# Kernel optimization log

Measured on AMD Instinct MI355X. Metric: run time of the kernel, lower is better.

## Reference

```python
import jax, jax.numpy as jnp
import numpy as np

B, T, I, H = 128, 1024, 128, 512


def setup_inputs():
    key = jax.random.key(0)
    ks = jax.random.split(key, 7)
    x = jax.random.normal(ks[0], (B, T, I), jnp.float32)
    mask = (jax.random.uniform(ks[1], (B, T)) < 0.1).astype(jnp.int32)
    # lengths sorted DESCENDING (required by the per-step batch truncation); max == T
    length = jnp.sort(jax.random.randint(ks[2], (B,), T // 2, T + 1))[::-1]
    length = length.at[0].set(T)
    s = 1.0 / np.sqrt(H)
    W_ih = jax.random.uniform(ks[3], (4 * H, I), jnp.float32, -s, s)
    W_hh = jax.random.uniform(ks[4], (4 * H, H), jnp.float32, -s, s)
    b_ih = jax.random.uniform(ks[5], (4 * H,), jnp.float32, -s, s)
    b_hh = jax.random.uniform(ks[6], (4 * H,), jnp.float32, -s, s)
    return dict(input=x, mask=mask, length=length, W_ih=W_ih, W_hh=W_hh, b_ih=b_ih, b_hh=b_hh)


def _boundary_mask(mask, length):
    # mask[:,0]=0 then scatter 1 at end index (length-1), as in the torch code
    Bq = mask.shape[0]
    m = mask.astype(jnp.float32)
    m = m.at[:, 0].set(0.0)
    m = m.at[jnp.arange(Bq), length - 1].set(1.0)
    return m


def _gather_index(m):
    # Replicates the pad-to-max-words while-loop + nonzero/gather pipeline.
    # The loop extends a suffix of ones until each row has exactly max_w ones;
    # equivalently: set to 1 every position whose suffix zero-count <= (max_w - num).
    Bq, Tq = m.shape
    word_nums = m.sum(axis=1)
    max_w = word_nums.max()
    need = max_w - word_nums
    zcum = jnp.cumsum((1.0 - m)[:, ::-1], axis=1)[:, ::-1]  # zeros in suffix (inclusive)
    padded = jnp.where(zcum <= need[:, None], 1.0, m)
    K = int(max_w)  # every row now has exactly K ones
    # column indices of the ones, in ascending order (row-major nonzero order)
    cols = jnp.argsort(1.0 - padded, axis=1, stable=True)[:, :K]
    # index = row*T + col - 1, gathered from the flattened embeddings (torch wraps -1)
    flat_idx = (jnp.arange(Bq)[:, None] * Tq + cols - 1) % (Bq * Tq)
    return flat_idx, word_nums, K


def _run_lstm(x, m, active, W_ih, W_hh, b_ih, b_hh):
    # Masked per-timestep LSTMCell: h,c are zeroed at boundaries (mask==0) before
    # each step; rows with t >= length are frozen (emulates batch_size_t truncation
    # for descending-sorted lengths) and their embeddings stay zero.
    Bq = x.shape[0]
    Hq = W_hh.shape[1]
    h0 = jnp.zeros((Bq, Hq), x.dtype)

    def step(carry, xs):
        h, c = carry
        x_t, m_t, a_t = xs
        h = h * m_t[:, None]
        c = c * m_t[:, None]
        gates = x_t @ W_ih.T + h @ W_hh.T + b_ih + b_hh
        i, f, g, o = jnp.split(gates, 4, axis=1)  # torch gate order i,f,g,o
        c2 = jax.nn.sigmoid(f) * c + jax.nn.sigmoid(i) * jnp.tanh(g)
        h2 = jax.nn.sigmoid(o) * jnp.tanh(c2)
        a = a_t[:, None]
        return (a * h2 + (1.0 - a) * h, a * c2 + (1.0 - a) * c), a * h2

    _, emb = jax.lax.scan(step, (h0, h0), (x.transpose(1, 0, 2), m.T, active.T))
    return emb.transpose(1, 0, 2)  # [B, T, H]


def reference(input, mask, length, W_ih, W_hh, b_ih, b_hh):
    Bq, Tq, _ = input.shape
    Hq = W_hh.shape[1]
    m = _boundary_mask(mask, length)
    active = (jnp.arange(Tq)[None, :] < length[:, None]).astype(input.dtype)
    emb = _run_lstm(input, m, active, W_ih, W_hh, b_ih, b_hh)
    flat_idx, word_nums, K = _gather_index(m)
    out = emb.reshape(Bq * Tq, Hq)[flat_idx]  # [B, K, H]
    return out, word_nums
```

## Files before the change

### kernel.cpp

```cpp
#include <hip/hip_runtime.h>
#include <math.h>

#define BB 128
#define TT 1024
#define II 128
#define HH 512
#define GG 2048
#define BT (BB*TT)
#define LMAX 10
#define NBUCK 12

#define BM 128
#define BN 128
#define KCH 128

typedef unsigned short u16;
typedef __attribute__((ext_vector_type(4))) u16 u16x4;
typedef __attribute__((ext_vector_type(8))) u16 u16x8;
typedef __attribute__((ext_vector_type(8))) short bf16x8;
typedef __attribute__((ext_vector_type(4))) float f32x4;

typedef __attribute__((address_space(3))) unsigned int lds_u32;
typedef __attribute__((address_space(1))) const unsigned int gbl_u32;

__device__ __forceinline__ void gload16(const void* g, void* l) {
    __builtin_amdgcn_global_load_lds((gbl_u32*)g, (lds_u32*)l, 16, 0, 0);
}

__device__ __forceinline__ float rcpf(float x) { return __builtin_amdgcn_rcpf(x); }
__device__ __forceinline__ float sigf(float v) { return rcpf(1.0f + __expf(-v)); }
__device__ __forceinline__ float tanhfast(float x) {
    float e = __expf(2.0f * x);
    return 1.0f - 2.0f * rcpf(e + 1.0f);
}

__device__ __forceinline__ u16 f2b(float f) {
    unsigned int x = __float_as_uint(f);
    return (u16)((x + 0x7fffu + ((x >> 16) & 1u)) >> 16);
}

__host__ __device__ __forceinline__ void buck_geom(int bkt, int CAP0, int* off, int* cap) {
    if (bkt == 0) { *off = 0; *cap = CAP0; return; }
    int o = CAP0;
    if (bkt == 1) { *off = o; *cap = 2048; return; } o += 2048;
    if (bkt == 2) { *off = o; *cap = 2048; return; } o += 2048;
    if (bkt == 3) { *off = o; *cap = 512;  return; } o += 512;
    if (bkt == 4) { *off = o; *cap = 128;  return; } o += 128;
    *off = o + (bkt - 5) * 64; *cap = 64;
}
#define LIST_EXTRA (2048 + 2048 + 512 + 128 + 7*64)

__device__ __forceinline__ int block_scan_excl(int* ws4, int tid, int v, int* total) {
    int lane = tid & 63, wv = tid >> 6;
    int incl = v;
#pragma unroll
    for (int s = 1; s < 64; s <<= 1) {
        int u = __shfl_up(incl, (unsigned)s, 64);
        if (lane >= s) incl += u;
    }
    __syncthreads();
    if (lane == 63) ws4[wv] = incl;
    __syncthreads();
    int base = 0, tot = 0;
#pragma unroll
    for (int i = 0; i < 4; ++i) { int t = ws4[i]; if (i < wv) base += t; tot += t; }
    *total = tot;
    return base + incl - v;
}

__global__ void k_wcvt(const float* __restrict__ Wih, const float* __restrict__ Whh,
                       u16* __restrict__ wihb, u16* __restrict__ whhb,
                       int* __restrict__ levelCount) {
    if (blockIdx.x == 0 && threadIdx.x < NBUCK) levelCount[threadIdx.x] = 0;
    int i = blockIdx.x * 256 + threadIdx.x;
    const int NW = GG * II / 4;
    const int NH = GG * HH / 4;
    if (i < NW) {
        float4 v = ((const float4*)Wih)[i];
        u16x4 u = { f2b(v.x), f2b(v.y), f2b(v.z), f2b(v.w) };
        ((u16x4*)wihb)[i] = u;
    } else if (i < NW + NH) {
        int j = i - NW;
        float4 v = ((const float4*)Whh)[j];
        u16x4 u = { f2b(v.x), f2b(v.y), f2b(v.z), f2b(v.w) };
        ((u16x4*)whhb)[j] = u;
    }
}

__global__ __launch_bounds__(256) void k_prep(
    const int* __restrict__ mask, const int* __restrict__ length,
    const float* __restrict__ x, float* __restrict__ wnOut,
    int* __restrict__ levelCount, int2* __restrict__ levelList,
    int* __restrict__ slotOf, u16* __restrict__ xb, float* __restrict__ out,
    int K, int R, int CAP0) {
    __shared__ unsigned char sm[TT];
    __shared__ unsigned char sne[TT];
    __shared__ u16 sgp[TT];
    __shared__ int ws4[4];
    __shared__ int cnt[NBUCK], cnt2[NBUCK], bas[NBUCK];
    __shared__ u16 spos[256];
    __shared__ u16 zlist[256];
    __shared__ int zn;

    int b = blockIdx.x, tid = threadIdx.x;
    int len = length[b];
    int t0 = tid * 4;
    if (tid == 0) zn = 0;

    int4 mk = ((const int4*)(mask + (size_t)b * TT))[tid];
    int mraw[4] = { mk.x, mk.y, mk.z, mk.w };
    unsigned char mv[4];
    int lzero = 0;
#pragma unroll
    for (int j = 0; j < 4; ++j) {
        int t = t0 + j;
        unsigned char m = (t == len - 1) ? 1 : ((t == 0) ? 0 : (mraw[j] != 0));
        mv[j] = m;
        sm[t] = m;
        sgp[t] = 0;
        lzero += !m;
    }

    int Z;
    int zbase = block_scan_excl(ws4, tid, lzero, &Z);
    int wn = TT - Z;
    if (tid == 0) wnOut[b] = (float)wn;
    int need = K - wn;

    int psel[4];
    int lpad = 0;
    {
        int zb = zbase;
#pragma unroll
        for (int j = 0; j < 4; ++j) {
            int sel = mv[j] | ((Z - zb) <= need ? 1 : 0);
            psel[j] = sel;
            lpad += sel;
            zb += !mv[j];
        }
    }
    int ptot;
    int pbase = block_scan_excl(ws4, tid, lpad, &ptot);
    {
        int k = pbase;
#pragma unroll
        for (int j = 0; j < 4; ++j) {
            int t = t0 + j;
            if (psel[j]) {
                sgp[t - 1] = (u16)(k + 1);
                if (t - 1 >= len) {
                    int zi = atomicAdd(&zn, 1);
                    if (zi < 256) zlist[zi] = (u16)k;
                }
                ++k;
            }
        }
    }
    __syncthreads();

    int nev[4], lvlv[4];
    int lne = 0;
#pragma unroll
    for (int j = 0; j < 4; ++j) {
        int t = t0 + j;
        int ne = 0;
        if (t < len) {
            int tt = t;
            ne = sgp[tt] != 0;
            while (!ne && tt + 1 < TT && tt + 1 < len && sm[tt + 1]) { ++tt; ne = sgp[tt] != 0; }
        }
        nev[j] = ne;
        sne[t] = (unsigned char)ne;
        lne += ne;
        int l = 0;
        if (mv[j]) { int tt = t; while (tt >= 0 && sm[tt] && l < LMAX - 1) { ++l; --tt; } }
        lvlv[j] = l;
    }

    int ntot;
    int nbase = block_scan_excl(ws4, tid, lne, &ntot);
    {
        int r = nbase;
        int sv[4];
#pragma unroll
        for (int j = 0; j < 4; ++j) {
            if (nev[j]) { sv[j] = b * R + r; if (r < 256) spos[r] = (u16)(t0 + j); }
            else sv[j] = -1;
            r += nev[j];
        }
        *(int4*)(slotOf + (size_t)b * TT + t0) = make_int4(sv[0], sv[1], sv[2], sv[3]);
    }

    if (tid < NBUCK) { cnt[tid] = 0; cnt2[tid] = 0; }
    __syncthreads();
    int bktv[4];
#pragma unroll
    for (int j = 0; j < 4; ++j) {
        bktv[j] = -1;
        if (nev[j]) {
            int t = t0 + j;
            int pred = (t + 1 < TT) && sm[t + 1] && sne[t + 1];
            int bkt = pred ? (2 + lvlv[j]) : (lvlv[j] ? 1 : 0);
            bktv[j] = bkt;
            atomicAdd(&cnt[bkt], 1);
        }
    }
    __syncthreads();
    if (tid < NBUCK) bas[tid] = cnt[tid] ? atomicAdd(&levelCount[tid], cnt[tid]) : 0;
    __syncthreads();
#pragma unroll
    for (int j = 0; j < 4; ++j) if (nev[j]) {
        int t = t0 + j;
        int bkt = bktv[j];
        int r = atomicAdd(&cnt2[bkt], 1);
        int off, cap;
        buck_geom(bkt, CAP0, &off, &cap);
        int idx = bas[bkt] + r;
        unsigned int y = ((bkt >= 2) ? 0x80000000u : 0u) | (unsigned int)sgp[t];
        if (idx < cap) levelList[off + idx] = make_int2(b * TT + t, (int)y);
    }
    __syncthreads();

    int nv = (ntot < 256 ? ntot : 256) * 16;
    for (int idx = tid; idx < nv; idx += 256) {
        int r = idx >> 4, part = idx & 15;
        int t = spos[r];
        const float* src = x + ((size_t)b * TT + t) * II + part * 8;
        float4 v0 = ((const float4*)src)[0];
        float4 v1 = ((const float4*)src)[1];
        u16x8 u = { f2b(v0.x), f2b(v0.y), f2b(v0.z), f2b(v0.w),
                    f2b(v1.x), f2b(v1.y), f2b(v1.z), f2b(v1.w) };
        *(u16x8*)(xb + ((size_t)b * R + r) * II + part * 8) = u;
    }
    int znv = zn < 256 ? zn : 256;
    for (int idx = tid; idx < znv * 128; idx += 256) {
        int e = idx >> 7, q = idx & 127;
        ((float4*)(out + ((size_t)b * K + zlist[e]) * HH))[q] = make_float4(0.f, 0.f, 0.f, 0.f);
    }
}

template<int HASH>
__device__ __forceinline__ void gemm_tile(
    const int2* __restrict__ list, int nrow, int jg,
    const u16* __restrict__ xb, const u16* __restrict__ wihb, const u16* __restrict__ whhb,
    const float* __restrict__ bih, const float* __restrict__ bhh,
    const int* __restrict__ slotOf, u16* __restrict__ hb, float* __restrict__ cbuf,
    float* __restrict__ out, int K,
    u16* As, u16* Bs, int* sSlot, int* sPrev, int* sAux) {
    int tid = threadIdx.x;
    if (tid < BM) {
        int2 e = list[(tid < nrow) ? tid : 0];
        int pos = e.x;
        sSlot[tid] = slotOf[pos];
        sPrev[tid] = HASH ? slotOf[pos - 1] : 0;
        unsigned int y = (unsigned int)e.y;
        int grank = (int)(y & 0xFFFFu);
        sAux[tid] = (int)((y & 0x80000000u) | (unsigned int)(grank ? ((pos >> 10) * K + grank) : 0));
    }
    __syncthreads();

    int w = tid >> 6, l = tid & 63;
    int lrow = l >> 4;
    int cbyte = (l & 15) << 4;
    f32x4 acc[2][8];
#pragma unroll
    for (int rb = 0; rb < 2; ++rb)
#pragma unroll
        for (int cb = 0; cb < 8; ++cb) acc[rb][cb] = (f32x4)0.f;

    const int nch = HASH ? 5 : 1;
    for (int kc = 0; kc < nch; ++kc) {
        bool fromX = (kc == 0);
        int koff = kc * KCH - II;
#pragma unroll
        for (int i = 0; i < 8; ++i) {
            int rr = (w << 5) + (i << 2) + lrow;
            int so = cbyte ^ ((rr & 7) << 4);
            const char* srcA = fromX
                ? (const char*)(xb + (size_t)sSlot[rr] * II) + so
                : (const char*)(hb + (size_t)sPrev[rr] * HH + koff) + so;
            gload16(srcA, (char*)As + (w << 13) + (i << 10));
            int gj = (rr >> 5) * HH + jg * 32 + (rr & 31);
            const char* srcB = fromX
                ? (const char*)(wihb + (size_t)gj * II) + so
                : (const char*)(whhb + (size_t)gj * HH + koff) + so;
            gload16(srcB, (char*)Bs + (w << 13) + (i << 10));
        }
        __syncthreads();
#pragma unroll
        for (int s = 0; s < 4; ++s) {
            bf16x8 af[2], bfr[8];
#pragma unroll
            for (int rb = 0; rb < 2; ++rb) {
                int rr = w * 32 + rb * 16 + (l & 15);
                int byte = rr * 256 + ((s * 64 + (l >> 4) * 16) ^ ((rr & 7) << 4));
                af[rb] = *(const bf16x8*)((const char*)As + byte);
            }
#pragma unroll
            for (int cb = 0; cb < 8; ++cb) {
                int rr = cb * 16 + (l & 15);
                int byte = rr * 256 + ((s * 64 + (l >> 4) * 16) ^ ((rr & 7) << 4));
                bfr[cb] = *(const bf16x8*)((const char*)Bs + byte);
            }
#pragma unroll
            for (int rb = 0; rb < 2; ++rb)
#pragma unroll
                for (int cb = 0; cb < 8; ++cb)
                    acc[rb][cb] = __builtin_amdgcn_mfma_f32_16x16x32_bf16(
                        af[rb], bfr[cb], acc[rb][cb], 0, 0, 0);
        }
        __syncthreads();
    }

    int u = l & 15;
    int h0 = jg * 32 + u;
    float b_i[2], b_f[2], b_g[2], b_o[2];
#pragma unroll
    for (int h = 0; h < 2; ++h) {
        int hc = h0 + h * 16;
        b_i[h] = bih[hc] + bhh[hc];
        b_f[h] = bih[HH + hc] + bhh[HH + hc];
        b_g[h] = bih[2 * HH + hc] + bhh[2 * HH + hc];
        b_o[h] = bih[3 * HH + hc] + bhh[3 * HH + hc];
    }
#pragma unroll
    for (int rb = 0; rb < 2; ++rb) {
#pragma unroll
        for (int r = 0; r < 4; ++r) {
            int m = w * 32 + rb * 16 + (l >> 4) * 4 + r;
            if (m < nrow) {
                int aux = sAux[m];
                int oi = aux & 0x7FFFFFFF;
                int sp = HASH ? sPrev[m] : 0;
                int sl = sSlot[m];
#pragma unroll
                for (int h = 0; h < 2; ++h) {
                    int hc = h0 + h * 16;
                    float gi = acc[rb][0 + h][r] + b_i[h];
                    float gf = acc[rb][2 + h][r] + b_f[h];
                    float gg = acc[rb][4 + h][r] + b_g[h];
                    float go = acc[rb][6 + h][r] + b_o[h];
                    float cin = HASH ? cbuf[(size_t)sp * HH + hc] : 0.f;
                    float c2 = sigf(gf) * cin + sigf(gi) * tanhfast(gg);
                    float h2 = sigf(go) * tanhfast(c2);
                    if (oi) out[(size_t)(oi - 1) * HH + hc] = h2;
                    if (aux < 0) {
                        hb[(size_t)sl * HH + hc] = f2b(h2);
                        cbuf[(size_t)sl * HH + hc] = c2;
                    }
                }
            }
        }
    }
}

template<int HASH>
__global__ __launch_bounds__(256) void k_gemm(
    int cntIdx, int listOff, int cap,
    const int* __restrict__ levelCount, const int2* __restrict__ levelList,
    const u16* __restrict__ xb, const u16* __restrict__ wihb, const u16* __restrict__ whhb,
    const float* __restrict__ bih, const float* __restrict__ bhh,
    const int* __restrict__ slotOf, u16* __restrict__ hb, float* __restrict__ cbuf,
    float* __restrict__ out, int K) {
    __shared__ __align__(16) u16 As[BM * KCH];
    __shared__ __align__(16) u16 Bs[BN * KCH];
    __shared__ int sSlot[BM], sPrev[BM], sAux[BM];
    int n = levelCount[cntIdx];
    if (n > cap) n = cap;
    int base = blockIdx.x * BM;
    if (base >= n) return;
    gemm_tile<HASH>(levelList + listOff + base, min(BM, n - base), blockIdx.y,
                    xb, wihb, whhb, bih, bhh, slotOf, hb, cbuf, out, K,
                    As, Bs, sSlot, sPrev, sAux);
}

__global__ __launch_bounds__(256) void k_big0(
    int offS, int capS, int CAP0,
    const int* __restrict__ levelCount, const int2* __restrict__ levelList,
    const u16* __restrict__ xb, const u16* __restrict__ wihb, const u16* __restrict__ whhb,
    const float* __restrict__ bih, const float* __restrict__ bhh,
    const int* __restrict__ slotOf, u16* __restrict__ hb, float* __restrict__ cbuf,
    float* __restrict__ out, int K) {
    __shared__ __align__(16) u16 As[BM * KCH];
    __shared__ __align__(16) u16 Bs[BN * KCH];
    __shared__ int sSlot[BM], sPrev[BM], sAux[BM];
    int ntS = capS / BM;
    int bx = blockIdx.x;
    const int2* lst;
    int n, base;
    if (bx < ntS) {
        n = levelCount[2]; if (n > capS) n = capS;
        base = bx * BM;
        lst = levelList + offS;
    } else {
        n = levelCount[0]; if (n > CAP0) n = CAP0;
        base = (bx - ntS) * BM;
        lst = levelList;
    }
    if (base >= n) return;
    gemm_tile<0>(lst + base, min(BM, n - base), blockIdx.y,
                 xb, wihb, whhb, bih, bhh, slotOf, hb, cbuf, out, K,
                 As, Bs, sSlot, sPrev, sAux);
}

extern "C" void kernel_launch(void* const* d_in, const int* in_sizes, int n_in,
                              void* d_out, int out_size, void* d_ws, size_t ws_size,
                              hipStream_t stream) {
    const float* x    = (const float*)d_in[0];
    const int* mask   = (const int*)d_in[1];
    const int* length = (const int*)d_in[2];
    const float* Wih  = (const float*)d_in[3];
    const float* Whh  = (const float*)d_in[4];
    const float* bih  = (const float*)d_in[5];
    const float* bhh  = (const float*)d_in[6];
    float* out = (float*)d_out;

    int K = (out_size - BB) / (BB * HH);
    int R = K + 64;
    int SLOTS = BB * R;
    int CAP0 = SLOTS;

    char* basep = (char*)d_ws;
    size_t off = 0;
    auto take = [&](size_t bytes) -> char* {
        off = (off + 255) & ~(size_t)255;
        char* p = basep + off;
        off += bytes;
        return p;
    };
    int* slotOf      = (int*)take((size_t)BT * 4);
    int* levelCount  = (int*)take(NBUCK * 4);
    int2* levelList  = (int2*)take((size_t)(CAP0 + LIST_EXTRA) * 8);
    u16* xb          = (u16*)take((size_t)SLOTS * II * 2);
    u16* hb          = (u16*)take((size_t)SLOTS * HH * 2);
    float* cbuf      = (float*)take((size_t)SLOTS * HH * 4);
    u16* wihb        = (u16*)take((size_t)GG * II * 2);
    u16* whhb        = (u16*)take((size_t)GG * HH * 2);
    (void)ws_size; (void)in_sizes; (void)n_in;

    k_wcvt<<<(GG * (II + HH) / 4 + 255) / 256, 256, 0, stream>>>(Wih, Whh, wihb, whhb, levelCount);
    k_prep<<<BB, 256, 0, stream>>>(mask, length, x, out + (size_t)BB * K * HH,
                                   levelCount, levelList, slotOf, xb, out, K, R, CAP0);

    int off_, cap_;
    buck_geom(2, CAP0, &off_, &cap_);
    {
        int ntS = cap_ / BM;
        int nt0 = (CAP0 + BM - 1) / BM;
        k_big0<<<dim3(ntS + nt0, GG / BN), 256, 0, stream>>>(
            off_, cap_, CAP0, levelCount, levelList, xb, wihb, whhb, bih, bhh,
            slotOf, hb, cbuf, out, K);
    }
    buck_geom(3, CAP0, &off_, &cap_);
    k_gemm<1><<<dim3(cap_ / BM, GG / BN), 256, 0, stream>>>(
        3, off_, cap_, levelCount, levelList, xb, wihb, whhb, bih, bhh,
        slotOf, hb, cbuf, out, K);
    for (int lev = 2; lev <= 9; ++lev) {
        buck_geom(2 + lev, CAP0, &off_, &cap_);
        k_gemm<1><<<dim3(1, GG / BN), 256, 0, stream>>>(
            2 + lev, off_, cap_, levelCount, levelList, xb, wihb, whhb, bih, bhh,
            slotOf, hb, cbuf, out, K);
    }
    buck_geom(1, CAP0, &off_, &cap_);
    k_gemm<1><<<dim3(cap_ / BM, GG / BN), 256, 0, stream>>>(
        1, off_, cap_, levelCount, levelList, xb, wihb, whhb, bih, bhh,
        slotOf, hb, cbuf, out, K);
}
```

Before: 97.81 us.

## Split buckets by level, pair launches, fuse weight conversion, grid-barrier tail levels

Weight bf16 conversion moves into extra blocks of the prep kernel, and counter zeroing moves to a memset. Non-successor entries are now bucketed by chain level, so each level's successor and non-successor rows are handled together in one dual-list launch. Levels 5-9 are processed in a single persistent kernel that uses an atomic spin barrier across its 32 blocks. The goal is fewer small kernel launches and less per-launch serialization. The cost is a spin barrier that relies on all 32 blocks being co-resident, plus more bucket bookkeeping.

```diff
diff --git a/kernel.cpp b/kernel.cpp
--- a/kernel.cpp
+++ b/kernel.cpp
@@ -8,7 +8,7 @@
 #define GG 2048
 #define BT (BB*TT)
 #define LMAX 10
-#define NBUCK 12
+#define NBUCK 20
 
 #define BM 128
 #define BN 128
@@ -39,16 +39,23 @@
     return (u16)((x + 0x7fffu + ((x >> 16) & 1u)) >> 16);
 }
 
-__host__ __device__ __forceinline__ void buck_geom(int bkt, int CAP0, int* off, int* cap) {
-    if (bkt == 0) { *off = 0; *cap = CAP0; return; }
-    int o = CAP0;
-    if (bkt == 1) { *off = o; *cap = 2048; return; } o += 2048;
-    if (bkt == 2) { *off = o; *cap = 2048; return; } o += 2048;
-    if (bkt == 3) { *off = o; *cap = 512;  return; } o += 512;
-    if (bkt == 4) { *off = o; *cap = 128;  return; } o += 128;
-    *off = o + (bkt - 5) * 64; *cap = 64;
-}
-#define LIST_EXTRA (2048 + 2048 + 512 + 128 + 7*64)
+__host__ __device__ __forceinline__ int buck_cap(int bkt, int CAP0) {
+    if (bkt == 0) return CAP0;
+    if (bkt == 1) return 2048;
+    if (bkt == 2) return 256;
+    if (bkt == 3) return 128;
+    if (bkt <= 9) return 64;
+    if (bkt == 10) return 2048;
+    if (bkt == 11) return 512;
+    if (bkt == 12) return 128;
+    return 64;
+}
+__host__ __device__ __forceinline__ int buck_off(int bkt, int CAP0) {
+    int o = 0;
+    for (int i = 0; i < bkt; ++i) o += buck_cap(i, CAP0);
+    return o;
+}
+#define LIST_EXTRA (2048 + 256 + 128 + 6*64 + 2048 + 512 + 128 + 7*64)
 
 __device__ __forceinline__ int block_scan_excl(int* ws4, int tid, int v, int* total) {
     int lane = tid & 63, wv = tid >> 6;
@@ -66,25 +73,6 @@
     for (int i = 0; i < 4; ++i) { int t = ws4[i]; if (i < wv) base += t; tot += t; }
     *total = tot;
     return base + incl - v;
-}
-
-__global__ void k_wcvt(const float* __restrict__ Wih, const float* __restrict__ Whh,
-                       u16* __restrict__ wihb, u16* __restrict__ whhb,
-                       int* __restrict__ levelCount) {
-    if (blockIdx.x == 0 && threadIdx.x < NBUCK) levelCount[threadIdx.x] = 0;
-    int i = blockIdx.x * 256 + threadIdx.x;
-    const int NW = GG * II / 4;
-    const int NH = GG * HH / 4;
-    if (i < NW) {
-        float4 v = ((const float4*)Wih)[i];
-        u16x4 u = { f2b(v.x), f2b(v.y), f2b(v.z), f2b(v.w) };
-        ((u16x4*)wihb)[i] = u;
-    } else if (i < NW + NH) {
-        int j = i - NW;
-        float4 v = ((const float4*)Whh)[j];
-        u16x4 u = { f2b(v.x), f2b(v.y), f2b(v.z), f2b(v.w) };
-        ((u16x4*)whhb)[j] = u;
-    }
 }
 
 __global__ __launch_bounds__(256) void k_prep(
@@ -92,20 +80,41 @@
     const float* __restrict__ x, float* __restrict__ wnOut,
     int* __restrict__ levelCount, int2* __restrict__ levelList,
     int* __restrict__ slotOf, u16* __restrict__ xb, float* __restrict__ out,
+    const float* __restrict__ Wih, const float* __restrict__ Whh,
+    u16* __restrict__ wihb, u16* __restrict__ whhb,
     int K, int R, int CAP0) {
+    int tid = threadIdx.x;
+    if (blockIdx.x >= BB) {
+        int i = (blockIdx.x - BB) * 256 + tid;
+        const int NW = GG * II / 4;
+        const int NH = GG * HH / 4;
+        if (i < NW) {
+            float4 v = ((const float4*)Wih)[i];
+            u16x4 u = { f2b(v.x), f2b(v.y), f2b(v.z), f2b(v.w) };
+            ((u16x4*)wihb)[i] = u;
+        } else if (i < NW + NH) {
+            int j = i - NW;
+            float4 v = ((const float4*)Whh)[j];
+            u16x4 u = { f2b(v.x), f2b(v.y), f2b(v.z), f2b(v.w) };
+            ((u16x4*)whhb)[j] = u;
+        }
+        return;
+    }
+
     __shared__ unsigned char sm[TT];
     __shared__ unsigned char sne[TT];
     __shared__ u16 sgp[TT];
     __shared__ int ws4[4];
-    __shared__ int cnt[NBUCK], cnt2[NBUCK], bas[NBUCK];
+    __shared__ int cnt[NBUCK], cnt2[NBUCK], bas[NBUCK], boff[NBUCK];
     __shared__ u16 spos[256];
     __shared__ u16 zlist[256];
     __shared__ int zn;
 
-    int b = blockIdx.x, tid = threadIdx.x;
+    int b = blockIdx.x;
     int len = length[b];
     int t0 = tid * 4;
     if (tid == 0) zn = 0;
+    if (tid < NBUCK) { cnt[tid] = 0; cnt2[tid] = 0; boff[tid] = buck_off(tid, CAP0); }
 
     int4 mk = ((const int4*)(mask + (size_t)b * TT))[tid];
     int mraw[4] = { mk.x, mk.y, mk.z, mk.w };
@@ -190,9 +199,8 @@
         }
         *(int4*)(slotOf + (size_t)b * TT + t0) = make_int4(sv[0], sv[1], sv[2], sv[3]);
     }
-
-    if (tid < NBUCK) { cnt[tid] = 0; cnt2[tid] = 0; }
-    __syncthreads();
+    __syncthreads();
+
     int bktv[4];
 #pragma unroll
     for (int j = 0; j < 4; ++j) {
@@ -200,7 +208,7 @@
         if (nev[j]) {
             int t = t0 + j;
             int pred = (t + 1 < TT) && sm[t + 1] && sne[t + 1];
-            int bkt = pred ? (2 + lvlv[j]) : (lvlv[j] ? 1 : 0);
+            int bkt = pred ? (10 + lvlv[j]) : lvlv[j];
             bktv[j] = bkt;
             atomicAdd(&cnt[bkt], 1);
         }
@@ -213,11 +221,9 @@
         int t = t0 + j;
         int bkt = bktv[j];
         int r = atomicAdd(&cnt2[bkt], 1);
-        int off, cap;
-        buck_geom(bkt, CAP0, &off, &cap);
         int idx = bas[bkt] + r;
-        unsigned int y = ((bkt >= 2) ? 0x80000000u : 0u) | (unsigned int)sgp[t];
-        if (idx < cap) levelList[off + idx] = make_int2(b * TT + t, (int)y);
+        unsigned int y = ((bkt >= 10) ? 0x80000000u : 0u) | (unsigned int)sgp[t];
+        if (idx < buck_cap(bkt, CAP0)) levelList[boff[bkt] + idx] = make_int2(b * TT + t, (int)y);
     }
     __syncthreads();
 
@@ -309,7 +315,7 @@
                     acc[rb][cb] = __builtin_amdgcn_mfma_f32_16x16x32_bf16(
                         af[rb], bfr[cb], acc[rb][cb], 0, 0, 0);
         }
-        __syncthreads();
+        if (kc + 1 < nch) __syncthreads();
     }
 
     int u = l & 15;
@@ -355,8 +361,8 @@
 }
 
 template<int HASH>
-__global__ __launch_bounds__(256) void k_gemm(
-    int cntIdx, int listOff, int cap,
+__global__ __launch_bounds__(256) void k_dual(
+    int bktA, int offA, int capA, int bktB, int offB, int capB,
     const int* __restrict__ levelCount, const int2* __restrict__ levelList,
     const u16* __restrict__ xb, const u16* __restrict__ wihb, const u16* __restrict__ whhb,
     const float* __restrict__ bih, const float* __restrict__ bhh,
@@ -365,42 +371,65 @@
     __shared__ __align__(16) u16 As[BM * KCH];
     __shared__ __align__(16) u16 Bs[BN * KCH];
     __shared__ int sSlot[BM], sPrev[BM], sAux[BM];
-    int n = levelCount[cntIdx];
-    if (n > cap) n = cap;
-    int base = blockIdx.x * BM;
+    int ntA = (capA + BM - 1) / BM;
+    int bx = blockIdx.x;
+    const int2* lst;
+    int n, base;
+    if (bx < ntA) {
+        n = levelCount[bktA]; if (n > capA) n = capA;
+        base = bx * BM;
+        lst = levelList + offA;
+    } else {
+        n = levelCount[bktB]; if (n > capB) n = capB;
+        base = (bx - ntA) * BM;
+        lst = levelList + offB;
+    }
     if (base >= n) return;
-    gemm_tile<HASH>(levelList + listOff + base, min(BM, n - base), blockIdx.y,
+    gemm_tile<HASH>(lst + base, min(BM, n - base), blockIdx.y,
                     xb, wihb, whhb, bih, bhh, slotOf, hb, cbuf, out, K,
                     As, Bs, sSlot, sPrev, sAux);
 }
 
-__global__ __launch_bounds__(256) void k_big0(
-    int offS, int capS, int CAP0,
-    const int* __restrict__ levelCount, const int2* __restrict__ levelList,
+__global__ __launch_bounds__(256) void k_tail59(
+    int CAP0, const int* __restrict__ levelCount, const int2* __restrict__ levelList,
     const u16* __restrict__ xb, const u16* __restrict__ wihb, const u16* __restrict__ whhb,
     const float* __restrict__ bih, const float* __restrict__ bhh,
     const int* __restrict__ slotOf, u16* __restrict__ hb, float* __restrict__ cbuf,
-    float* __restrict__ out, int K) {
+    float* __restrict__ out, int K, int* __restrict__ bar) {
     __shared__ __align__(16) u16 As[BM * KCH];
     __shared__ __align__(16) u16 Bs[BN * KCH];
     __shared__ int sSlot[BM], sPrev[BM], sAux[BM];
-    int ntS = capS / BM;
-    int bx = blockIdx.x;
-    const int2* lst;
-    int n, base;
-    if (bx < ntS) {
-        n = levelCount[2]; if (n > capS) n = capS;
-        base = bx * BM;
-        lst = levelList + offS;
-    } else {
-        n = levelCount[0]; if (n > CAP0) n = CAP0;
-        base = (bx - ntS) * BM;
-        lst = levelList;
-    }
-    if (base >= n) return;
-    gemm_tile<0>(lst + base, min(BM, n - base), blockIdx.y,
-                 xb, wihb, whhb, bih, bhh, slotOf, hb, cbuf, out, K,
-                 As, Bs, sSlot, sPrev, sAux);
+    int tid = threadIdx.x;
+    int iter = 0;
+    for (int l = 5; l <= 9; ++l) {
+        int bkt = (blockIdx.x == 0) ? (10 + l) : l;
+        int cap = buck_cap(bkt, CAP0);
+        int n = levelCount[bkt]; if (n > cap) n = cap;
+        if (n > 0) {
+            gemm_tile<1>(levelList + buck_off(bkt, CAP0), min(BM, n), blockIdx.y,
+                         xb, wihb, whhb, bih, bhh, slotOf, hb, cbuf, out, K,
+                         As, Bs, sSlot, sPrev, sAux);
+        }
+        int rem = 0;
+        for (int j = l + 1; j <= 9; ++j) {
+            int a = levelCount[10 + j]; if (a > buck_cap(10 + j, CAP0)) a = buck_cap(10 + j, CAP0);
+            int c = levelCount[j];      if (c > buck_cap(j, CAP0))      c = buck_cap(j, CAP0);
+            rem += a + c;
+        }
+        ++iter;
+        if (rem == 0) return;
+        __threadfence();
+        __syncthreads();
+        if (tid == 0) {
+            __hip_atomic_fetch_add(bar, 1, __ATOMIC_RELEASE, __HIP_MEMORY_SCOPE_AGENT);
+            int target = 32 * iter;
+            while (__hip_atomic_load(bar, __ATOMIC_ACQUIRE, __HIP_MEMORY_SCOPE_AGENT) < target) {
+                __builtin_amdgcn_s_sleep(1);
+            }
+        }
+        __syncthreads();
+        __threadfence();
+    }
 }
 
 extern "C" void kernel_launch(void* const* d_in, const int* in_sizes, int n_in,
@@ -429,40 +458,39 @@
         return p;
     };
     int* slotOf      = (int*)take((size_t)BT * 4);
-    int* levelCount  = (int*)take(NBUCK * 4);
+    int* levelCount  = (int*)take((NBUCK + 1) * 4);
     int2* levelList  = (int2*)take((size_t)(CAP0 + LIST_EXTRA) * 8);
     u16* xb          = (u16*)take((size_t)SLOTS * II * 2);
     u16* hb          = (u16*)take((size_t)SLOTS * HH * 2);
     float* cbuf      = (float*)take((size_t)SLOTS * HH * 4);
     u16* wihb        = (u16*)take((size_t)GG * II * 2);
     u16* whhb        = (u16*)take((size_t)GG * HH * 2);
+    int* bar         = levelCount + NBUCK;
     (void)ws_size; (void)in_sizes; (void)n_in;
 
-    k_wcvt<<<(GG * (II + HH) / 4 + 255) / 256, 256, 0, stream>>>(Wih, Whh, wihb, whhb, levelCount);
-    k_prep<<<BB, 256, 0, stream>>>(mask, length, x, out + (size_t)BB * K * HH,
-                                   levelCount, levelList, slotOf, xb, out, K, R, CAP0);
-
-    int off_, cap_;
-    buck_geom(2, CAP0, &off_, &cap_);
+    hipMemsetAsync(levelCount, 0, (NBUCK + 1) * 4, stream);
+
+    const int NWCVT = (GG * (II + HH) / 4 + 255) / 256;
+    k_prep<<<BB + NWCVT, 256, 0, stream>>>(
+        mask, length, x, out + (size_t)BB * K * HH,
+        levelCount, levelList, slotOf, xb, out, Wih, Whh, wihb, whhb, K, R, CAP0);
+
     {
-        int ntS = cap_ / BM;
-        int nt0 = (CAP0 + BM - 1) / BM;
-        k_big0<<<dim3(ntS + nt0, GG / BN), 256, 0, stream>>>(
-            off_, cap_, CAP0, levelCount, levelList, xb, wihb, whhb, bih, bhh,
-            slotOf, hb, cbuf, out, K);
-    }
-    buck_geom(3, CAP0, &off_, &cap_);
-    k_gemm<1><<<dim3(cap_ / BM, GG / BN), 256, 0, stream>>>(
-        3, off_, cap_, levelCount, levelList, xb, wihb, whhb, bih, bhh,
-        slotOf, hb, cbuf, out, K);
-    for (int lev = 2; lev <= 9; ++lev) {
-        buck_geom(2 + lev, CAP0, &off_, &cap_);
-        k_gemm<1><<<dim3(1, GG / BN), 256, 0, stream>>>(
-            2 + lev, off_, cap_, levelCount, levelList, xb, wihb, whhb, bih, bhh,
-            slotOf, hb, cbuf, out, K);
-    }
-    buck_geom(1, CAP0, &off_, &cap_);
-    k_gemm<1><<<dim3(cap_ / BM, GG / BN), 256, 0, stream>>>(
-        1, off_, cap_, levelCount, levelList, xb, wihb, whhb, bih, bhh,
-        slotOf, hb, cbuf, out, K);
-}
+        int oS = buck_off(10, CAP0), cS = buck_cap(10, CAP0);
+        int ntS = (cS + BM - 1) / BM, ntL = (CAP0 + BM - 1) / BM;
+        k_dual<0><<<dim3(ntS + ntL, GG / BN), 256, 0, stream>>>(
+            10, oS, cS, 0, 0, CAP0, levelCount, levelList,
+            xb, wihb, whhb, bih, bhh, slotOf, hb, cbuf, out, K);
+    }
+    for (int l = 1; l <= 4; ++l) {
+        int oS = buck_off(10 + l, CAP0), cS = buck_cap(10 + l, CAP0);
+        int oL = buck_off(l, CAP0),      cL = buck_cap(l, CAP0);
+        int ntS = (cS + BM - 1) / BM, ntL = (cL + BM - 1) / BM;
+        k_dual<1><<<dim3(ntS + ntL, GG / BN), 256, 0, stream>>>(
+            10 + l, oS, cS, l, oL, cL, levelCount, levelList,
+            xb, wihb, whhb, bih, bhh, slotOf, hb, cbuf, out, K);
+    }
+    k_tail59<<<dim3(2, GG / BN), 256, 0, stream>>>(
+        CAP0, levelCount, levelList, xb, wihb, whhb, bih, bhh,
+        slotOf, hb, cbuf, out, K, bar);
+}
```

After: 95.25 us. 2.6% less time.
